# Kernel tuning notes

Measured on AMD Instinct MI355X. Metric: run time of the kernel, lower is better.

The kernel has to match this reference:

```python
import jax, jax.numpy as jnp
import numpy as np

N_HEADS = 16
ATT_DIM = 1024
HEAD_DIM = ATT_DIM // N_HEADS
SCALE = 1.0 / (HEAD_DIM ** 0.5)


def setup_inputs() -> dict:
    key = jax.random.key(0)
    k1, k2 = jax.random.split(key)
    B, N, D = 4, 2048, 1024
    X = jax.random.normal(k1, (B, N, D), dtype=jnp.float32)
    W_qkv = jax.random.normal(k2, (3 * ATT_DIM, D), dtype=jnp.float32) * 0.02  # trunc_normal-ish std
    return {"X": X, "W_qkv": W_qkv}


def reference(X, W_qkv):
    B, N, D = X.shape
    # qkv projection (bias=False): X @ W^T -> [b, n, 3*att_dim]
    QKV = jnp.einsum('bnd,od->bno', X, W_qkv)
    # rearrange 'b n (p h d) -> p b h n d'
    QKV = QKV.reshape(B, N, 3, N_HEADS, HEAD_DIM).transpose(2, 0, 3, 1, 4)
    Q, K, V = QKV[0], QKV[1], QKV[2]
    # scaled dot-product attention, full NxN scores (as in source)
    scores = jnp.einsum('bhid,bhjd->bhij', Q, K) * SCALE
    S = jax.nn.softmax(scores, axis=-1)
    # dropout rate is 0.0 -> identity
    Y = jnp.einsum('bhij,bhjd->bhid', S, V)
    # 'b h n d -> b n (h d)'; out_proj is Identity (out_dim == att_dim)
    return Y.transpose(0, 2, 1, 3).reshape(B, N, N_HEADS * HEAD_DIM)
```

## Files before the change

### kernel.cpp

```cpp
#include <hip/hip_runtime.h>

#define BATCH   4
#define SEQ     2048
#define DMODEL  1024
#define NHEADS  16
#define HDIM    64
#define QSC     0.18033688f

typedef short s16x8 __attribute__((ext_vector_type(8)));
typedef float f32x4 __attribute__((ext_vector_type(4)));
typedef const __attribute__((address_space(1))) unsigned int* gas_t;
typedef __attribute__((address_space(3))) unsigned int* las_t;

__device__ inline unsigned short f2bf(float f) {
    unsigned int u = __float_as_uint(f);
    u += 0x7FFF + ((u >> 16) & 1);
    return (unsigned short)(u >> 16);
}

__device__ __forceinline__ float exp2_fast(float x) {
#if __has_builtin(__builtin_amdgcn_exp2f)
    return __builtin_amdgcn_exp2f(x);
#else
    return exp2f(x);
#endif
}

__device__ __forceinline__ float rcp_fast(float x) {
#if __has_builtin(__builtin_amdgcn_rcpf)
    return __builtin_amdgcn_rcpf(x);
#else
    return 1.0f / x;
#endif
}

__device__ __forceinline__ unsigned int pack_bf16x2(float lo, float hi) {
    unsigned int a = __float_as_uint(lo) + 0x8000u;
    unsigned int b = __float_as_uint(hi) + 0x8000u;
#if __has_builtin(__builtin_amdgcn_perm)
    return __builtin_amdgcn_perm(b, a, 0x07060302u);
#else
    return (a >> 16) | (b & 0xFFFF0000u);
#endif
}

__global__ void cvt_bf16(const float* __restrict__ in,
                         unsigned short* __restrict__ out, int n4) {
    int i = blockIdx.x * blockDim.x + threadIdx.x;
    if (i >= n4) return;
    float4 v = ((const float4*)in)[i];
    ushort4 o;
    o.x = f2bf(v.x); o.y = f2bf(v.y); o.z = f2bf(v.z); o.w = f2bf(v.w);
    ((ushort4*)out)[i] = o;
}

__global__ __launch_bounds__(256) void qkv_gemm(
    const unsigned short* __restrict__ Xb,
    const unsigned short* __restrict__ Wb,
    unsigned short* __restrict__ Qo,
    unsigned short* __restrict__ Ko,
    unsigned short* __restrict__ Vt)
{
    __shared__ __align__(16) unsigned short As[128 * 32];
    __shared__ __align__(16) unsigned short Bs[128 * 32];

    const int t    = threadIdx.x;
    const int m0   = blockIdx.y * 128;
    const int n0   = blockIdx.x * 128;
    const int wid  = t >> 6;
    const int lane = t & 63;
    const int l15  = lane & 15;
    const int quad = lane >> 4;
    const int wm   = (wid >> 1) * 64;
    const int wn   = (wid & 1) * 64;

    const int srow = t >> 1;
    const int koff = (t & 1) * 16;

    f32x4 acc[4][4] = {};

    for (int k0 = 0; k0 < 1024; k0 += 32) {
        __syncthreads();
        {
            const uint4* ga = (const uint4*)&Xb[(size_t)(m0 + srow) * 1024 + k0 + koff];
            uint4* sa = (uint4*)&As[srow * 32 + koff];
            sa[0] = ga[0]; sa[1] = ga[1];
            const uint4* gb = (const uint4*)&Wb[(size_t)(n0 + srow) * 1024 + k0 + koff];
            uint4* sb = (uint4*)&Bs[srow * 32 + koff];
            sb[0] = gb[0]; sb[1] = gb[1];
        }
        __syncthreads();

        s16x8 af[4], bf[4];
        #pragma unroll
        for (int mt = 0; mt < 4; mt++)
            af[mt] = *(const s16x8*)&As[(wm + mt * 16 + l15) * 32 + quad * 8];
        #pragma unroll
        for (int nt = 0; nt < 4; nt++)
            bf[nt] = *(const s16x8*)&Bs[(wn + nt * 16 + l15) * 32 + quad * 8];
        #pragma unroll
        for (int mt = 0; mt < 4; mt++)
            #pragma unroll
            for (int nt = 0; nt < 4; nt++)
                acc[mt][nt] = __builtin_amdgcn_mfma_f32_16x16x32_bf16(
                    af[mt], bf[nt], acc[mt][nt], 0, 0, 0);
    }

    #pragma unroll
    for (int mt = 0; mt < 4; mt++) {
        const int mbase = m0 + wm + mt * 16 + quad * 4;
        const int b     = mbase >> 11;
        const int nbase = mbase & 2047;
        #pragma unroll
        for (int nt = 0; nt < 4; nt++) {
            const int o  = n0 + wn + nt * 16 + l15;
            const int p  = o >> 10;
            const int oo = o & 1023;
            const int h  = oo >> 6;
            const int d  = oo & 63;
            if (p == 0) {
                #pragma unroll
                for (int r = 0; r < 4; r++)
                    Qo[((size_t)(b * 16 + h) * 2048 + nbase + r) * 64 + d] =
                        f2bf(acc[mt][nt][r] * QSC);
            } else if (p == 1) {
                #pragma unroll
                for (int r = 0; r < 4; r++)
                    Ko[((size_t)(b * 16 + h) * 2048 + nbase + r) * 64 + d] =
                        f2bf(acc[mt][nt][r]);
            } else {
                ushort4 v4;
                v4.x = f2bf(acc[mt][nt][0]);
                v4.y = f2bf(acc[mt][nt][1]);
                v4.z = f2bf(acc[mt][nt][2]);
                v4.w = f2bf(acc[mt][nt][3]);
                *(ushort4*)&Vt[((size_t)(b * 16 + h) * 64 + d) * 2048 + nbase] = v4;
            }
        }
    }
}

#define PSTRIDE 72
#define PBASE   16384

__global__ __launch_bounds__(256) void attn(
    const unsigned short* __restrict__ Q,
    const unsigned short* __restrict__ K,
    const unsigned short* __restrict__ Vt,
    float* __restrict__ out)
{
    __shared__ __align__(16) unsigned short LDS[PBASE + 4 * 32 * PSTRIDE];

    const int t    = threadIdx.x;
    const int w    = t >> 6;
    const int lane = t & 63;
    const int l15  = lane & 15;
    const int quad = lane >> 4;
    const int head = blockIdx.y;
    const int b    = head >> 4;
    const int h    = head & 15;
    const int q0   = blockIdx.x * 128 + w * 32;

    const unsigned short* Qh = Q  + (size_t)head * 2048 * 64;
    const unsigned short* Kh = K  + (size_t)head * 2048 * 64;
    const unsigned short* Vh = Vt + (size_t)head * 64 * 2048;

    const int r0 = t >> 3;
    const int c0 = (t & 7) ^ (r0 & 7);
    const unsigned short* srcK = Kh + r0 * 64 + c0 * 8;
    const unsigned short* srcV = Vh + r0 * 2048 + c0 * 8;

    auto stageKV = [&](int kt, int bufE) {
        #pragma unroll
        for (int rd = 0; rd < 2; rd++) {
            __builtin_amdgcn_global_load_lds(
                (gas_t)(const void*)(srcK + kt * 4096 + rd * 2048),
                (las_t)(void*)&LDS[bufE + rd * 2048 + w * 512], 16, 0, 0);
            __builtin_amdgcn_global_load_lds(
                (gas_t)(const void*)(srcV + kt * 64 + rd * 65536),
                (las_t)(void*)&LDS[bufE + 4096 + rd * 2048 + w * 512], 16, 0, 0);
        }
    };

    s16x8 qb[2][2];
    #pragma unroll
    for (int mt = 0; mt < 2; mt++)
        #pragma unroll
        for (int kc = 0; kc < 2; kc++)
            qb[mt][kc] = *(const s16x8*)&Qh[(size_t)(q0 + mt * 16 + l15) * 64 + kc * 32 + quad * 8];

    f32x4 y[2][4] = {};
    float lsum[2] = {0.f, 0.f};
    unsigned short* P = &LDS[PBASE + w * (32 * PSTRIDE)];

    const int x7   = l15 & 7;
    const int csw0 = (quad ^ x7) * 8;
    const int csw1 = ((4 + quad) ^ x7) * 8;

    auto compute = [&](int bufE) {
        s16x8 kb[4][2];
        #pragma unroll
        for (int nt = 0; nt < 4; nt++) {
            const int rowb = bufE + (nt * 16 + l15) * 64;
            kb[nt][0] = *(const s16x8*)&LDS[rowb + csw0];
            kb[nt][1] = *(const s16x8*)&LDS[rowb + csw1];
        }
        f32x4 st[4][2] = {};
        #pragma unroll
        for (int kc = 0; kc < 2; kc++)
            #pragma unroll
            for (int nt = 0; nt < 4; nt++)
                #pragma unroll
                for (int mt = 0; mt < 2; mt++)
                    st[nt][mt] = __builtin_amdgcn_mfma_f32_16x16x32_bf16(
                        kb[nt][kc], qb[mt][kc], st[nt][mt], 0, 0, 0);
        s16x8 vb[4][2];
        #pragma unroll
        for (int dt = 0; dt < 4; dt++) {
            const int rowb = bufE + 4096 + (dt * 16 + l15) * 64;
            vb[dt][0] = *(const s16x8*)&LDS[rowb + csw0];
            vb[dt][1] = *(const s16x8*)&LDS[rowb + csw1];
        }
        #pragma unroll
        for (int mt = 0; mt < 2; mt++)
            #pragma unroll
            for (int nt = 0; nt < 4; nt++) {
                float p0 = exp2_fast(st[nt][mt][0]);
                float p1 = exp2_fast(st[nt][mt][1]);
                float p2 = exp2_fast(st[nt][mt][2]);
                float p3 = exp2_fast(st[nt][mt][3]);
                lsum[mt] += (p0 + p1) + (p2 + p3);
                uint2 u;
                u.x = pack_bf16x2(p0, p1);
                u.y = pack_bf16x2(p2, p3);
                *(uint2*)&P[(mt * 16 + l15) * PSTRIDE + nt * 16 + quad * 4] = u;
            }
        #pragma unroll
        for (int kc = 0; kc < 2; kc++) {
            s16x8 pa[2];
            #pragma unroll
            for (int mt = 0; mt < 2; mt++)
                pa[mt] = *(const s16x8*)&P[(mt * 16 + l15) * PSTRIDE + kc * 32 + quad * 8];
            #pragma unroll
            for (int mt = 0; mt < 2; mt++)
                #pragma unroll
                for (int dt = 0; dt < 4; dt++)
                    y[mt][dt] = __builtin_amdgcn_mfma_f32_16x16x32_bf16(
                        pa[mt], vb[dt][kc], y[mt][dt], 0, 0, 0);
        }
    };

    stageKV(0, 0);
    __syncthreads();

    #pragma unroll 1
    for (int kt = 0; kt < 32; kt += 2) {
        stageKV(kt + 1, 8192);
        compute(0);
        __syncthreads();
        if (kt + 2 < 32) stageKV(kt + 2, 0);
        compute(8192);
        __syncthreads();
    }

    #pragma unroll
    for (int mt = 0; mt < 2; mt++) {
        float v = lsum[mt];
        v += __shfl_xor(v, 16);
        v += __shfl_xor(v, 32);
        lsum[mt] = v;
    }

    float rinv[2][4];
    #pragma unroll
    for (int mt = 0; mt < 2; mt++)
        #pragma unroll
        for (int r = 0; r < 4; r++)
            rinv[mt][r] = rcp_fast(__shfl(lsum[mt], quad * 4 + r));

    #pragma unroll
    for (int mt = 0; mt < 2; mt++)
        #pragma unroll
        for (int dt = 0; dt < 4; dt++)
            #pragma unroll
            for (int r = 0; r < 4; r++) {
                const int n = q0 + mt * 16 + quad * 4 + r;
                const int d = dt * 16 + l15;
                out[((size_t)(b * 2048 + n)) * 1024 + h * 64 + d] =
                    y[mt][dt][r] * rinv[mt][r];
            }
}

extern "C" void kernel_launch(void* const* d_in, const int* in_sizes, int n_in,
                              void* d_out, int out_size, void* d_ws, size_t ws_size,
                              hipStream_t stream) {
    const float* X = (const float*)d_in[0];
    const float* W = (const float*)d_in[1];
    float* out = (float*)d_out;

    char* ws = (char*)d_ws;
    unsigned short* Xb = (unsigned short*)(ws);
    unsigned short* Wb = (unsigned short*)(ws + 16777216);
    unsigned short* Qb = (unsigned short*)(ws + 23068672);
    unsigned short* Kb = (unsigned short*)(ws + 39845888);
    unsigned short* Vt = (unsigned short*)(ws + 56623104);

    cvt_bf16<<<dim3(8192), dim3(256), 0, stream>>>(X, Xb, 2097152);
    cvt_bf16<<<dim3(3072), dim3(256), 0, stream>>>(W, Wb, 786432);
    qkv_gemm<<<dim3(24, 64), dim3(256), 0, stream>>>(Xb, Wb, Qb, Kb, Vt);
    attn<<<dim3(16, 64), dim3(256), 0, stream>>>(Qb, Kb, Vt, out);
}
```

Baseline: 266.0 us.

## Double-buffer QKV GEMM via registers and single-buffer attention K/V staging

The QKV GEMM now prefetches the next K-slab into registers while the MFMAs run, writes it to a second LDS buffer, and needs one barrier per iteration instead of two. The attention kernel drops its double-buffered K/V LDS to a single buffer, halving LDS use and adding a launch-bounds occupancy hint of 4 blocks. The next tile is issued after K/V fragments are loaded to registers. The GEMM epilogue is also rewritten to per-element stores, which turns the former vectorised V-transpose store into scalar stores. The attention change trades load/compute overlap for higher occupancy.

Measured after the change: 266.3 us. No clear change (+0.1%).

```diff
diff --git a/kernel.cpp b/kernel.cpp
--- a/kernel.cpp
+++ b/kernel.cpp
@@ -54,15 +54,15 @@
     ((ushort4*)out)[i] = o;
 }
 
-__global__ __launch_bounds__(256) void qkv_gemm(
+__global__ __launch_bounds__(256, 4) void qkv_gemm(
     const unsigned short* __restrict__ Xb,
     const unsigned short* __restrict__ Wb,
     unsigned short* __restrict__ Qo,
     unsigned short* __restrict__ Ko,
     unsigned short* __restrict__ Vt)
 {
-    __shared__ __align__(16) unsigned short As[128 * 32];
-    __shared__ __align__(16) unsigned short Bs[128 * 32];
+    __shared__ __align__(16) unsigned short As[2][128 * 32];
+    __shared__ __align__(16) unsigned short Bs[2][128 * 32];
 
     const int t    = threadIdx.x;
     const int m0   = blockIdx.y * 128;
@@ -77,40 +77,57 @@
     const int srow = t >> 1;
     const int koff = (t & 1) * 16;
 
+    const unsigned short* gA = &Xb[(size_t)(m0 + srow) * 1024 + koff];
+    const unsigned short* gB = &Wb[(size_t)(n0 + srow) * 1024 + koff];
+
     f32x4 acc[4][4] = {};
-
+    uint4 ra0, ra1, rb0, rb1;
+
+    auto gload = [&](int k0) {
+        const uint4* pa = (const uint4*)(gA + k0);
+        ra0 = pa[0]; ra1 = pa[1];
+        const uint4* pb = (const uint4*)(gB + k0);
+        rb0 = pb[0]; rb1 = pb[1];
+    };
+    auto swrite = [&](int buf) {
+        uint4* sa = (uint4*)&As[buf][srow * 32 + koff];
+        sa[0] = ra0; sa[1] = ra1;
+        uint4* sb = (uint4*)&Bs[buf][srow * 32 + koff];
+        sb[0] = rb0; sb[1] = rb1;
+    };
+
+    gload(0);
+    swrite(0);
+    __syncthreads();
+
+    int cur = 0;
+    #pragma unroll 1
     for (int k0 = 0; k0 < 1024; k0 += 32) {
-        __syncthreads();
-        {
-            const uint4* ga = (const uint4*)&Xb[(size_t)(m0 + srow) * 1024 + k0 + koff];
-            uint4* sa = (uint4*)&As[srow * 32 + koff];
-            sa[0] = ga[0]; sa[1] = ga[1];
-            const uint4* gb = (const uint4*)&Wb[(size_t)(n0 + srow) * 1024 + k0 + koff];
-            uint4* sb = (uint4*)&Bs[srow * 32 + koff];
-            sb[0] = gb[0]; sb[1] = gb[1];
-        }
-        __syncthreads();
+        const bool more = (k0 + 32) < 1024;
+        if (more) gload(k0 + 32);
 
         s16x8 af[4], bf[4];
         #pragma unroll
         for (int mt = 0; mt < 4; mt++)
-            af[mt] = *(const s16x8*)&As[(wm + mt * 16 + l15) * 32 + quad * 8];
+            af[mt] = *(const s16x8*)&As[cur][(wm + mt * 16 + l15) * 32 + quad * 8];
         #pragma unroll
         for (int nt = 0; nt < 4; nt++)
-            bf[nt] = *(const s16x8*)&Bs[(wn + nt * 16 + l15) * 32 + quad * 8];
+            bf[nt] = *(const s16x8*)&Bs[cur][(wn + nt * 16 + l15) * 32 + quad * 8];
         #pragma unroll
         for (int mt = 0; mt < 4; mt++)
             #pragma unroll
             for (int nt = 0; nt < 4; nt++)
                 acc[mt][nt] = __builtin_amdgcn_mfma_f32_16x16x32_bf16(
                     af[mt], bf[nt], acc[mt][nt], 0, 0, 0);
+
+        if (more) swrite(cur ^ 1);
+        __syncthreads();
+        cur ^= 1;
     }
 
     #pragma unroll
     for (int mt = 0; mt < 4; mt++) {
         const int mbase = m0 + wm + mt * 16 + quad * 4;
-        const int b     = mbase >> 11;
-        const int nbase = mbase & 2047;
         #pragma unroll
         for (int nt = 0; nt < 4; nt++) {
             const int o  = n0 + wn + nt * 16 + l15;
@@ -118,32 +135,27 @@
             const int oo = o & 1023;
             const int h  = oo >> 6;
             const int d  = oo & 63;
-            if (p == 0) {
-                #pragma unroll
-                for (int r = 0; r < 4; r++)
-                    Qo[((size_t)(b * 16 + h) * 2048 + nbase + r) * 64 + d] =
-                        f2bf(acc[mt][nt][r] * QSC);
-            } else if (p == 1) {
-                #pragma unroll
-                for (int r = 0; r < 4; r++)
-                    Ko[((size_t)(b * 16 + h) * 2048 + nbase + r) * 64 + d] =
-                        f2bf(acc[mt][nt][r]);
-            } else {
-                ushort4 v4;
-                v4.x = f2bf(acc[mt][nt][0]);
-                v4.y = f2bf(acc[mt][nt][1]);
-                v4.z = f2bf(acc[mt][nt][2]);
-                v4.w = f2bf(acc[mt][nt][3]);
-                *(ushort4*)&Vt[((size_t)(b * 16 + h) * 64 + d) * 2048 + nbase] = v4;
+            #pragma unroll
+            for (int r = 0; r < 4; r++) {
+                const int mm = mbase + r;
+                const int b  = mm >> 11;
+                const int n  = mm & 2047;
+                float v = acc[mt][nt][r];
+                if (p == 0)
+                    Qo[((size_t)(b * 16 + h) * 2048 + n) * 64 + d] = f2bf(v * QSC);
+                else if (p == 1)
+                    Ko[((size_t)(b * 16 + h) * 2048 + n) * 64 + d] = f2bf(v);
+                else
+                    Vt[((size_t)(b * 16 + h) * 64 + d) * 2048 + n] = f2bf(v);
             }
         }
     }
 }
 
 #define PSTRIDE 72
-#define PBASE   16384
-
-__global__ __launch_bounds__(256) void attn(
+#define PBASE   8192
+
+__global__ __launch_bounds__(256, 4) void attn(
     const unsigned short* __restrict__ Q,
     const unsigned short* __restrict__ K,
     const unsigned short* __restrict__ Vt,
@@ -170,15 +182,15 @@
     const unsigned short* srcK = Kh + r0 * 64 + c0 * 8;
     const unsigned short* srcV = Vh + r0 * 2048 + c0 * 8;
 
-    auto stageKV = [&](int kt, int bufE) {
+    auto stage = [&](int kt) {
         #pragma unroll
         for (int rd = 0; rd < 2; rd++) {
             __builtin_amdgcn_global_load_lds(
                 (gas_t)(const void*)(srcK + kt * 4096 + rd * 2048),
-                (las_t)(void*)&LDS[bufE + rd * 2048 + w * 512], 16, 0, 0);
+                (las_t)(void*)&LDS[rd * 2048 + w * 512], 16, 0, 0);
             __builtin_amdgcn_global_load_lds(
                 (gas_t)(const void*)(srcV + kt * 64 + rd * 65536),
-                (las_t)(void*)&LDS[bufE + 4096 + rd * 2048 + w * 512], 16, 0, 0);
+                (las_t)(void*)&LDS[4096 + rd * 2048 + w * 512], 16, 0, 0);
         }
     };
 
@@ -197,11 +209,15 @@
     const int csw0 = (quad ^ x7) * 8;
     const int csw1 = ((4 + quad) ^ x7) * 8;
 
-    auto compute = [&](int bufE) {
+    stage(0);
+    __syncthreads();
+
+    #pragma unroll 1
+    for (int kt = 0; kt < 32; kt++) {
         s16x8 kb[4][2];
         #pragma unroll
         for (int nt = 0; nt < 4; nt++) {
-            const int rowb = bufE + (nt * 16 + l15) * 64;
+            const int rowb = (nt * 16 + l15) * 64;
             kb[nt][0] = *(const s16x8*)&LDS[rowb + csw0];
             kb[nt][1] = *(const s16x8*)&LDS[rowb + csw1];
         }
@@ -214,13 +230,18 @@
                 for (int mt = 0; mt < 2; mt++)
                     st[nt][mt] = __builtin_amdgcn_mfma_f32_16x16x32_bf16(
                         kb[nt][kc], qb[mt][kc], st[nt][mt], 0, 0, 0);
+
         s16x8 vb[4][2];
         #pragma unroll
         for (int dt = 0; dt < 4; dt++) {
-            const int rowb = bufE + 4096 + (dt * 16 + l15) * 64;
+            const int rowb = 4096 + (dt * 16 + l15) * 64;
             vb[dt][0] = *(const s16x8*)&LDS[rowb + csw0];
             vb[dt][1] = *(const s16x8*)&LDS[rowb + csw1];
         }
+
+        __syncthreads();
+        if (kt + 1 < 32) stage(kt + 1);
+
         #pragma unroll
         for (int mt = 0; mt < 2; mt++)
             #pragma unroll
@@ -248,18 +269,7 @@
                     y[mt][dt] = __builtin_amdgcn_mfma_f32_16x16x32_bf16(
                         pa[mt], vb[dt][kc], y[mt][dt], 0, 0, 0);
         }
-    };
-
-    stageKV(0, 0);
-    __syncthreads();
-
-    #pragma unroll 1
-    for (int kt = 0; kt < 32; kt += 2) {
-        stageKV(kt + 1, 8192);
-        compute(0);
-        __syncthreads();
-        if (kt + 2 < 32) stageKV(kt + 2, 0);
-        compute(8192);
+
         __syncthreads();
     }
 
```
